# Performance work log

Measured on AMD Instinct MI355X. Metric: run time of the kernel, lower is better.

## Reference

```python
import jax, jax.numpy as jnp
import numpy as np

BN_EPS = 1e-3  # Keras BatchNormalization default epsilon


def setup_inputs() -> dict:
    key = jax.random.key(0)
    ks = jax.random.split(key, 10)
    B, H, W, F, K = 16, 64, 64, 512, 32
    support = 1.0 / np.sqrt(K * F)
    fc_support = np.sqrt(1.0 / F)
    return {
        "inputs": jax.random.normal(ks[0], (B, H, W, F), dtype=jnp.float32),
        # Encoder params
        "codewords": jax.random.uniform(ks[1], (K, F), minval=-support, maxval=support, dtype=jnp.float32),
        "smoothing": jax.random.uniform(ks[2], (K,), minval=-1.0, maxval=0.0, dtype=jnp.float32),
        # BatchNorm (inference mode: moving stats) over feature axis of (B, K, F)
        "bn_gamma": jnp.ones((F,), dtype=jnp.float32),
        "bn_beta": jnp.zeros((F,), dtype=jnp.float32),
        "bn_mean": jnp.zeros((F,), dtype=jnp.float32),
        "bn_var": jnp.ones((F,), dtype=jnp.float32),
        # Dense layers
        "fc_enc_w": jax.random.uniform(ks[3], (F, F), minval=-fc_support, maxval=fc_support, dtype=jnp.float32),
        "fc_enc_b": jax.random.uniform(ks[4], (F,), minval=-fc_support, maxval=fc_support, dtype=jnp.float32),
        "fc_se_w": jax.random.uniform(ks[5], (F, 1), minval=-fc_support, maxval=fc_support, dtype=jnp.float32),
        "fc_se_b": jax.random.uniform(ks[6], (1,), minval=-fc_support, maxval=fc_support, dtype=jnp.float32),
    }


def _encoder(x, codewords, smoothing, bn_gamma, bn_beta, bn_mean, bn_var):
    # x: (B, H, W, F) -> feats (B, N, F)
    B, H, W, F = x.shape
    feats = x.reshape(B, H * W, F)
    # Squared residual norms without materializing (B, N, K, F):
    x2 = jnp.sum(feats * feats, axis=-1, keepdims=True)          # (B, N, 1)
    c2 = jnp.sum(codewords * codewords, axis=-1)                 # (K,)
    xc = jnp.einsum("bnf,kf->bnk", feats, codewords)             # (B, N, K)
    sqnorms = x2 - 2.0 * xc + c2                                 # (B, N, K)
    s = jax.nn.softmax(sqnorms * smoothing, axis=-1)             # (B, N, K)
    # sum_n s[b,n,k] * (x[b,n] - c[k]) = s^T x - c * sum_n s
    s_sum = jnp.sum(s, axis=1)                                   # (B, K)
    enc = jnp.einsum("bnk,bnf->bkf", s, feats) - s_sum[:, :, None] * codewords  # (B, K, F)
    # BatchNorm (inference) + ReLU, then aggregate over codewords
    enc_bn = (enc - bn_mean) * jax.lax.rsqrt(bn_var + BN_EPS) * bn_gamma + bn_beta
    return jnp.sum(jax.nn.relu(enc_bn), axis=1)                  # (B, F)


def reference(inputs, codewords, smoothing, bn_gamma, bn_beta, bn_mean, bn_var,
              fc_enc_w, fc_enc_b, fc_se_w, fc_se_b):
    enc = _encoder(inputs, codewords, smoothing, bn_gamma, bn_beta, bn_mean, bn_var)
    attn = jax.nn.sigmoid(enc @ fc_enc_w + fc_enc_b)             # (B, F)
    featuremaps_out = attn[:, None, None, :] * inputs            # (B, H, W, F)
    se_loss_out = enc @ fc_se_w + fc_se_b                        # (B, 1)
    return (featuremaps_out, se_loss_out)
```

## Files before the change

kernel.cpp:

```cpp
#include <hip/hip_runtime.h>
#include <hip/hip_bf16.h>
#include <math.h>

#define Bb   16
#define HWn  4096
#define Ff   512
#define Kk   32
#define GCH  64

typedef __attribute__((ext_vector_type(8))) short  short8;
typedef __attribute__((ext_vector_type(4))) float  f32x4;

#define WS_SSUM  0
#define WS_EOUT  512
#define WS_ATTN  (WS_EOUT + Bb * Ff)
#define WS_CWB   (WS_ATTN + Bb * Ff)
#define WS_C2    (WS_CWB + 8192)
#define WS_SM    (WS_C2 + 32)

#define SCR_PART 0
#define SCR_RED  16777216

static __device__ __forceinline__ unsigned int pack2bf(float a, float b) {
    union { __hip_bfloat162 h; unsigned int u; } p;
    p.h = __float22bfloat162_rn(make_float2(a, b));
    return p.u;
}

__global__ void prep(const float* __restrict__ cw, const float* __restrict__ smth,
                     unsigned short* __restrict__ cwb,
                     float* __restrict__ c2l2, float* __restrict__ sml2)
{
    const int t = threadIdx.x;
    const float4* c4 = (const float4*)cw;
    #pragma unroll
    for (int j = 0; j < 16; ++j) {
        const int i = t + j * 256;
        const float4 v = c4[i];
        *reinterpret_cast<uint2*>(&cwb[i * 4]) =
            make_uint2(pack2bf(v.x, v.y), pack2bf(v.z, v.w));
    }
    const int k = t >> 3, sk = t & 7;
    float p = 0.f;
    #pragma unroll
    for (int j = 0; j < 16; ++j) {
        const float4 v = c4[k * 128 + sk + j * 8];
        p = fmaf(v.x, v.x, fmaf(v.y, v.y, fmaf(v.z, v.z, fmaf(v.w, v.w, p))));
    }
    p += __shfl_xor(p, 1); p += __shfl_xor(p, 2); p += __shfl_xor(p, 4);
    if (sk == 0) {
        const float L2E = 1.4426950408889634f;
        const float sm = smth[k];
        sml2[k] = sm * L2E;
        c2l2[k] = p * sm * L2E;
    }
}

__global__ __launch_bounds__(512, 2) void enc_fused(
    const float* __restrict__ x, const unsigned short* __restrict__ cwb,
    const float* __restrict__ c2l2, const float* __restrict__ sml2,
    float* __restrict__ part, float* __restrict__ s_sum)
{
    __shared__ __align__(16) float lgp[2][64][32];
    __shared__ float x2p[2][64];
    __shared__ float sm_s[32], c2_s[32];
    __shared__ float swred[8][32];

    const int tid  = threadIdx.x;
    const int wave = tid >> 6, lane = tid & 63;
    const int col  = lane & 15, g = lane >> 4;
    const int b    = blockIdx.y, cx = blockIdx.x;
    const int gr   = wave >> 1, fh = wave & 1;
    const int n_loc = gr * 16 + col;
    const int n     = cx * 64 + n_loc;

    if (tid < 32) { sm_s[tid] = sml2[tid]; c2_s[tid] = c2l2[tid]; }

    {
        const float4* xr = (const float4*)(x + ((size_t)b * HWn + n) * Ff) + fh * 64 + g * 2;
        const unsigned short* a0p = cwb + col * 512 + fh * 256 + g * 8;
        const unsigned short* a1p = a0p + 16 * 512;
        f32x4 c0 = {0.f, 0.f, 0.f, 0.f}, c1 = {0.f, 0.f, 0.f, 0.f};
        float px = 0.f;
        #pragma unroll
        for (int fs = 0; fs < 8; ++fs) {
            const float4 v0 = xr[fs * 8];
            const float4 v1 = xr[fs * 8 + 1];
            px = fmaf(v0.x, v0.x, fmaf(v0.y, v0.y, fmaf(v0.z, v0.z, fmaf(v0.w, v0.w, px))));
            px = fmaf(v1.x, v1.x, fmaf(v1.y, v1.y, fmaf(v1.z, v1.z, fmaf(v1.w, v1.w, px))));
            union { uint4 u; short8 s; } bu;
            bu.u = make_uint4(pack2bf(v0.x, v0.y), pack2bf(v0.z, v0.w),
                              pack2bf(v1.x, v1.y), pack2bf(v1.z, v1.w));
            const short8 a0 = *(const short8*)(a0p + fs * 32);
            const short8 a1 = *(const short8*)(a1p + fs * 32);
            c0 = __builtin_amdgcn_mfma_f32_16x16x32_bf16(a0, bu.s, c0, 0, 0, 0);
            c1 = __builtin_amdgcn_mfma_f32_16x16x32_bf16(a1, bu.s, c1, 0, 0, 0);
        }
        px += __shfl_xor(px, 16); px += __shfl_xor(px, 32);
        if (g == 0) x2p[fh][n_loc] = px;
        #pragma unroll
        for (int r = 0; r < 4; ++r) {
            lgp[fh][n_loc][g * 4 + r]      = c0[r];
            lgp[fh][n_loc][16 + g * 4 + r] = c1[r];
        }
    }
    __syncthreads();

    const int srow = tid >> 3, sf = tid & 7;
    float ssl[4];
    {
        const float x2v = x2p[0][srow] + x2p[1][srow];
        float lg[4];
        #pragma unroll
        for (int r = 0; r < 4; ++r) {
            const int k = sf * 4 + r;
            const float xc = lgp[0][srow][k] + lgp[1][srow][k];
            lg[r] = fmaf(sm_s[k], fmaf(-2.f, xc, x2v), c2_s[k]);
        }
        float m = fmaxf(fmaxf(lg[0], lg[1]), fmaxf(lg[2], lg[3]));
        m = fmaxf(m, __shfl_xor(m, 1));
        m = fmaxf(m, __shfl_xor(m, 2));
        m = fmaxf(m, __shfl_xor(m, 4));
        float e[4], sum = 0.f;
        #pragma unroll
        for (int r = 0; r < 4; ++r) { e[r] = exp2f(lg[r] - m); sum += e[r]; }
        sum += __shfl_xor(sum, 1); sum += __shfl_xor(sum, 2); sum += __shfl_xor(sum, 4);
        const float inv = 1.f / sum;
        #pragma unroll
        for (int r = 0; r < 4; ++r) {
            const float s = e[r] * inv;
            lgp[0][srow][sf * 4 + r] = s;
            ssl[r] = s;
        }
    }
    #pragma unroll
    for (int r = 0; r < 4; ++r) {
        float v = ssl[r];
        v += __shfl_xor(v, 8); v += __shfl_xor(v, 16); v += __shfl_xor(v, 32);
        if (lane < 8) swred[wave][lane * 4 + r] = v;
    }
    __syncthreads();
    if (tid < 32) {
        float a = 0.f;
        #pragma unroll
        for (int w = 0; w < 8; ++w) a += swred[w][tid];
        atomicAdd(&s_sum[b * Kk + tid], a);
    }

    float acc[4][8];
    #pragma unroll
    for (int j = 0; j < 4; ++j)
        #pragma unroll
        for (int i = 0; i < 8; ++i) acc[j][i] = 0.f;

    const int kq = wave * 4;
    const float* s_base = &lgp[0][0][0];
    const float4* xp = (const float4*)(x + ((size_t)b * HWn + cx * 64) * Ff) + lane * 2;
    #pragma unroll 4
    for (int nn = 0; nn < 64; ++nn) {
        const f32x4 sv = *(const f32x4*)&s_base[nn * 32 + kq];
        const float4 v0 = xp[nn * 128];
        const float4 v1 = xp[nn * 128 + 1];
        const float fx[8] = {v0.x, v0.y, v0.z, v0.w, v1.x, v1.y, v1.z, v1.w};
        #pragma unroll
        for (int j = 0; j < 4; ++j) {
            const float sj = sv[j];
            #pragma unroll
            for (int i = 0; i < 8; ++i)
                acc[j][i] = fmaf(sj, fx[i], acc[j][i]);
        }
    }
    float* basep = part + (size_t)(b * GCH + cx) * (Kk * Ff) +
                   (size_t)(wave * 4) * Ff + lane * 8;
    #pragma unroll
    for (int j = 0; j < 4; ++j) {
        *reinterpret_cast<float4*>(basep + j * Ff) =
            make_float4(acc[j][0], acc[j][1], acc[j][2], acc[j][3]);
        *reinterpret_cast<float4*>(basep + j * Ff + 4) =
            make_float4(acc[j][4], acc[j][5], acc[j][6], acc[j][7]);
    }
}

__global__ void enc_red(const float* __restrict__ scr, float* __restrict__ outp)
{
    const int idx = blockIdx.x * 256 + threadIdx.x;
    const int b   = idx >> 14;
    const int rem = idx & 16383;
    const float* p = scr + (size_t)b * GCH * 16384 + rem;
    float a = 0.f;
    #pragma unroll
    for (int c = 0; c < GCH; ++c) a += p[c * 16384];
    outp[idx] = a;
}

__global__ void enc_finish(const float* __restrict__ enc_acc,
                           const float* __restrict__ s_sum,
                           const float* __restrict__ cw,
                           const float* __restrict__ gamma,
                           const float* __restrict__ beta,
                           const float* __restrict__ mean,
                           const float* __restrict__ var,
                           const float* __restrict__ se_w,
                           const float* __restrict__ se_b,
                           float* __restrict__ enc_out,
                           float* __restrict__ se_out)
{
    __shared__ float ss[Kk];
    __shared__ float red[8];
    const int b = blockIdx.x, f = threadIdx.x;
    if (f < Kk) ss[f] = s_sum[b * Kk + f];
    __syncthreads();
    const float m  = mean[f];
    const float g  = gamma[f];
    const float bt = beta[f];
    const float iv = rsqrtf(var[f] + 1e-3f);
    float a = 0.f;
    #pragma unroll 4
    for (int k = 0; k < Kk; ++k) {
        float v = enc_acc[((long)b * Kk + k) * Ff + f] - ss[k] * cw[k * Ff + f];
        v = (v - m) * iv * g + bt;
        a += fmaxf(v, 0.f);
    }
    enc_out[b * Ff + f] = a;
    float p = a * se_w[f];
    p += __shfl_down(p, 32); p += __shfl_down(p, 16); p += __shfl_down(p, 8);
    p += __shfl_down(p, 4);  p += __shfl_down(p, 2);  p += __shfl_down(p, 1);
    if ((f & 63) == 0) red[f >> 6] = p;
    __syncthreads();
    if (f == 0) {
        float t = 0.f;
        #pragma unroll
        for (int i = 0; i < 8; ++i) t += red[i];
        se_out[b] = t + se_b[0];
    }
}

__global__ void attn_fc(const float* __restrict__ enc_out,
                        const float* __restrict__ W,
                        const float* __restrict__ bias,
                        float* __restrict__ attn)
{
    __shared__ float eo[Bb][Ff];
    const int t = threadIdx.x, fg = blockIdx.x;
    #pragma unroll
    for (int j = 0; j < 4; ++j)
        reinterpret_cast<float4*>(&eo[0][0])[t + j * 512] =
            reinterpret_cast<const float4*>(enc_out)[t + j * 512];
    __syncthreads();
    const int f  = fg * 64 + (t & 63);
    const int b0 = t >> 6;
    float a0 = bias[f], a1 = bias[f];
    #pragma unroll 8
    for (int fp = 0; fp < Ff; ++fp) {
        const float w = W[fp * Ff + f];
        a0 = fmaf(eo[b0][fp],     w, a0);
        a1 = fmaf(eo[b0 + 8][fp], w, a1);
    }
    attn[b0 * Ff + f]       = 1.f / (1.f + expf(-a0));
    attn[(b0 + 8) * Ff + f] = 1.f / (1.f + expf(-a1));
}

__global__ void bcast_mul(const float4* __restrict__ x4,
                          const float* __restrict__ attn,
                          float4* __restrict__ o4)
{
    const int stride = gridDim.x * blockDim.x;
    const int total4 = Bb * HWn * Ff / 4;
    for (int i = blockIdx.x * blockDim.x + threadIdx.x; i < total4; i += stride) {
        const float4 v = x4[i];
        const int f4 = i & 127;
        const int bb = i >> 19;
        const float4 a = *reinterpret_cast<const float4*>(&attn[bb * Ff + f4 * 4]);
        o4[i] = make_float4(v.x * a.x, v.y * a.y, v.z * a.z, v.w * a.w);
    }
}

extern "C" void kernel_launch(void* const* d_in, const int* in_sizes, int n_in,
                              void* d_out, int out_size, void* d_ws, size_t ws_size,
                              hipStream_t stream)
{
    (void)in_sizes; (void)n_in; (void)out_size; (void)ws_size;
    const float* x     = (const float*)d_in[0];
    const float* cw    = (const float*)d_in[1];
    const float* smth  = (const float*)d_in[2];
    const float* gamma = (const float*)d_in[3];
    const float* beta  = (const float*)d_in[4];
    const float* mean  = (const float*)d_in[5];
    const float* var   = (const float*)d_in[6];
    const float* Wenc  = (const float*)d_in[7];
    const float* benc  = (const float*)d_in[8];
    const float* Wse   = (const float*)d_in[9];
    const float* bse   = (const float*)d_in[10];

    float* out = (float*)d_out;
    float* ws  = (float*)d_ws;
    float* ssum = ws + WS_SSUM;
    float* eout = ws + WS_EOUT;
    float* attn = ws + WS_ATTN;
    unsigned short* cwb = (unsigned short*)(ws + WS_CWB);
    float* c2l2 = ws + WS_C2;
    float* sml2 = ws + WS_SM;

    float* scr_part = out + SCR_PART;
    float* scr_red  = out + SCR_RED;

    hipMemsetAsync(ssum, 0, (size_t)Bb * Kk * sizeof(float), stream);
    prep<<<1, 256, 0, stream>>>(cw, smth, cwb, c2l2, sml2);
    enc_fused<<<dim3(GCH, Bb), 512, 0, stream>>>(x, cwb, c2l2, sml2, scr_part, ssum);
    enc_red<<<1024, 256, 0, stream>>>(scr_part, scr_red);
    enc_finish<<<Bb, 512, 0, stream>>>(scr_red, ssum, cw, gamma, beta, mean, var,
                                       Wse, bse, eout, out + (long)Bb * HWn * Ff);
    attn_fc<<<8, 512, 0, stream>>>(eout, Wenc, benc, attn);
    bcast_mul<<<2048, 256, 0, stream>>>((const float4*)x, attn, (float4*)out);
}
```

Before: 191.5 us.

## Stage bf16 x tile in LDS and split MFMA logits by codeword half

```diff
diff --git a/kernel.cpp b/kernel.cpp
--- a/kernel.cpp
+++ b/kernel.cpp
@@ -61,8 +61,9 @@
     const float* __restrict__ c2l2, const float* __restrict__ sml2,
     float* __restrict__ part, float* __restrict__ s_sum)
 {
-    __shared__ __align__(16) float lgp[2][64][32];
-    __shared__ float x2p[2][64];
+    __shared__ __align__(16) unsigned short fb16[64 * 512];
+    __shared__ __align__(16) float lgx[64][36];
+    __shared__ float x2s[64];
     __shared__ float sm_s[32], c2_s[32];
     __shared__ float swred[8][32];
 
@@ -70,20 +71,18 @@
     const int wave = tid >> 6, lane = tid & 63;
     const int col  = lane & 15, g = lane >> 4;
     const int b    = blockIdx.y, cx = blockIdx.x;
-    const int gr   = wave >> 1, fh = wave & 1;
+    const int gr   = wave & 3, kh = wave >> 2;
     const int n_loc = gr * 16 + col;
-    const int n     = cx * 64 + n_loc;
 
     if (tid < 32) { sm_s[tid] = sml2[tid]; c2_s[tid] = c2l2[tid]; }
 
     {
-        const float4* xr = (const float4*)(x + ((size_t)b * HWn + n) * Ff) + fh * 64 + g * 2;
-        const unsigned short* a0p = cwb + col * 512 + fh * 256 + g * 8;
-        const unsigned short* a1p = a0p + 16 * 512;
-        f32x4 c0 = {0.f, 0.f, 0.f, 0.f}, c1 = {0.f, 0.f, 0.f, 0.f};
+        const float4* xr = (const float4*)(x + ((size_t)b * HWn + cx * 64 + n_loc) * Ff) + g * 2;
+        const unsigned short* ap = cwb + (kh * 16 + col) * 512 + g * 8;
+        f32x4 c0 = {0.f, 0.f, 0.f, 0.f};
         float px = 0.f;
         #pragma unroll
-        for (int fs = 0; fs < 8; ++fs) {
+        for (int fs = 0; fs < 16; ++fs) {
             const float4 v0 = xr[fs * 8];
             const float4 v1 = xr[fs * 8 + 1];
             px = fmaf(v0.x, v0.x, fmaf(v0.y, v0.y, fmaf(v0.z, v0.z, fmaf(v0.w, v0.w, px))));
@@ -91,31 +90,28 @@
             union { uint4 u; short8 s; } bu;
             bu.u = make_uint4(pack2bf(v0.x, v0.y), pack2bf(v0.z, v0.w),
                               pack2bf(v1.x, v1.y), pack2bf(v1.z, v1.w));
-            const short8 a0 = *(const short8*)(a0p + fs * 32);
-            const short8 a1 = *(const short8*)(a1p + fs * 32);
+            if (kh == 0) {
+                const int idx = n_loc * 512 + (((fs * 4 + g) ^ (n_loc & 7)) << 3);
+                *reinterpret_cast<uint4*>(&fb16[idx]) = bu.u;
+            }
+            const short8 a0 = *(const short8*)(ap + fs * 32);
             c0 = __builtin_amdgcn_mfma_f32_16x16x32_bf16(a0, bu.s, c0, 0, 0, 0);
-            c1 = __builtin_amdgcn_mfma_f32_16x16x32_bf16(a1, bu.s, c1, 0, 0, 0);
         }
         px += __shfl_xor(px, 16); px += __shfl_xor(px, 32);
-        if (g == 0) x2p[fh][n_loc] = px;
-        #pragma unroll
-        for (int r = 0; r < 4; ++r) {
-            lgp[fh][n_loc][g * 4 + r]      = c0[r];
-            lgp[fh][n_loc][16 + g * 4 + r] = c1[r];
-        }
+        if (kh == 0 && g == 0) x2s[n_loc] = px;
+        *reinterpret_cast<f32x4*>(&lgx[n_loc][kh * 16 + g * 4]) = c0;
     }
     __syncthreads();
 
     const int srow = tid >> 3, sf = tid & 7;
     float ssl[4];
     {
-        const float x2v = x2p[0][srow] + x2p[1][srow];
+        const float x2v = x2s[srow];
         float lg[4];
         #pragma unroll
         for (int r = 0; r < 4; ++r) {
             const int k = sf * 4 + r;
-            const float xc = lgp[0][srow][k] + lgp[1][srow][k];
-            lg[r] = fmaf(sm_s[k], fmaf(-2.f, xc, x2v), c2_s[k]);
+            lg[r] = fmaf(sm_s[k], fmaf(-2.f, lgx[srow][k], x2v), c2_s[k]);
         }
         float m = fmaxf(fmaxf(lg[0], lg[1]), fmaxf(lg[2], lg[3]));
         m = fmaxf(m, __shfl_xor(m, 1));
@@ -129,7 +125,7 @@
         #pragma unroll
         for (int r = 0; r < 4; ++r) {
             const float s = e[r] * inv;
-            lgp[0][srow][sf * 4 + r] = s;
+            lgx[srow][sf * 4 + r] = s;
             ssl[r] = s;
         }
     }
@@ -154,14 +150,19 @@
         for (int i = 0; i < 8; ++i) acc[j][i] = 0.f;
 
     const int kq = wave * 4;
-    const float* s_base = &lgp[0][0][0];
-    const float4* xp = (const float4*)(x + ((size_t)b * HWn + cx * 64) * Ff) + lane * 2;
     #pragma unroll 4
     for (int nn = 0; nn < 64; ++nn) {
-        const f32x4 sv = *(const f32x4*)&s_base[nn * 32 + kq];
-        const float4 v0 = xp[nn * 128];
-        const float4 v1 = xp[nn * 128 + 1];
-        const float fx[8] = {v0.x, v0.y, v0.z, v0.w, v1.x, v1.y, v1.z, v1.w};
+        const f32x4 sv = *(const f32x4*)&lgx[nn][kq];
+        const uint4 u = *(const uint4*)&fb16[nn * 512 + ((lane ^ (nn & 7)) << 3)];
+        float fx[8];
+        fx[0] = __uint_as_float(u.x << 16);
+        fx[1] = __uint_as_float(u.x & 0xffff0000u);
+        fx[2] = __uint_as_float(u.y << 16);
+        fx[3] = __uint_as_float(u.y & 0xffff0000u);
+        fx[4] = __uint_as_float(u.z << 16);
+        fx[5] = __uint_as_float(u.z & 0xffff0000u);
+        fx[6] = __uint_as_float(u.w << 16);
+        fx[7] = __uint_as_float(u.w & 0xffff0000u);
         #pragma unroll
         for (int j = 0; j < 4; ++j) {
             const float sj = sv[j];
```

After: 196.1 us. 1.02x slower.
